# Optimization experiments

Measured on AMD Instinct MI355X. Metric: run time of the kernel, lower is better.

Reference implementation:

```python
import jax, jax.numpy as jnp
import numpy as np

H = 1024
NUM_HEADS = 16
HEAD_DIM = H // NUM_HEADS
EPS = 1e-6
GEN_E, GEN_IE = 8, 4096 // 8     # general experts, per-expert intermediate
MOD_E, MOD_IE = 4, 4096 // 4     # per-modality experts, per-expert intermediate


def layernorm(x, g, b):
    m = jnp.mean(x, axis=-1, keepdims=True)
    v = jnp.mean((x - m) ** 2, axis=-1, keepdims=True)
    return (x - m) * jax.lax.rsqrt(v + EPS) * g + b


def attention(x, qkv_w, qkv_b, proj_w, proj_b):
    B, N, _ = x.shape
    qkv = (x @ qkv_w + qkv_b).reshape(B, N, 3, NUM_HEADS, HEAD_DIM)
    qkv = jnp.transpose(qkv, (2, 0, 3, 1, 4))  # [3,B,h,N,d]
    q, k, v = qkv[0], qkv[1], qkv[2]
    scale = HEAD_DIM ** -0.5
    attn = jax.nn.softmax(jnp.einsum('bhnd,bhmd->bhnm', q, k) * scale, axis=-1)
    out = jnp.einsum('bhnm,bhmd->bhnd', attn, v)
    out = jnp.transpose(out, (0, 2, 1, 3)).reshape(B, N, H)
    return out @ proj_w + proj_b


def routed_mlp(x, position_ids, gate_up, down, ie):
    # expert_id = position % num_experts; compute all experts then select per token
    # (avoids materializing per-token [T,H,2I] gathered weights).
    E = gate_up.shape[0]
    eids = position_ids % E  # [B,N]
    gu = jnp.einsum('bnh,ehi->bnei', x, gate_up)              # [B,N,E,2*ie]
    gu = jnp.take_along_axis(gu, eids[..., None, None], axis=2)[:, :, 0]
    gate, up = gu[..., :ie], gu[..., ie:]
    inter = jax.nn.silu(gate) * up                             # [B,N,ie]
    dn = jnp.einsum('bni,eih->bneh', inter, down)              # [B,N,E,H]
    return jnp.take_along_axis(dn, eids[..., None, None], axis=2)[:, :, 0]


def setup_inputs() -> dict:
    key = jax.random.key(0)
    ks = jax.random.split(key, 16)
    B, N = 2, 2048
    inp = {
        'x': jax.random.normal(ks[0], (B, N, H), jnp.float32),
        'qkv_w': jax.random.normal(ks[1], (H, 3 * H), jnp.float32) * 0.02,
        'qkv_b': jnp.zeros((3 * H,), jnp.float32),
        'proj_w': jax.random.normal(ks[2], (H, H), jnp.float32) * 0.02,
        'proj_b': jnp.zeros((H,), jnp.float32),
        'ln1_g': jnp.ones((H,), jnp.float32), 'ln1_b': jnp.zeros((H,), jnp.float32),
        'ln2_g': jnp.ones((H,), jnp.float32), 'ln2_b': jnp.zeros((H,), jnp.float32),
        'ln3_g': jnp.ones((H,), jnp.float32), 'ln3_b': jnp.zeros((H,), jnp.float32),
        'gen_gu': jax.random.normal(ks[3], (GEN_E, H, 2 * GEN_IE), jnp.float32) * 0.02,
        'gen_dn': jax.random.normal(ks[4], (GEN_E, GEN_IE, H), jnp.float32) * 0.02,
        'text_gu': jax.random.normal(ks[5], (MOD_E, H, 2 * MOD_IE), jnp.float32) * 0.02,
        'text_dn': jax.random.normal(ks[6], (MOD_E, MOD_IE, H), jnp.float32) * 0.02,
        'img_gu': jax.random.normal(ks[7], (MOD_E, H, 2 * MOD_IE), jnp.float32) * 0.02,
        'img_dn': jax.random.normal(ks[8], (MOD_E, MOD_IE, H), jnp.float32) * 0.02,
        'aud_gu': jax.random.normal(ks[9], (MOD_E, H, 2 * MOD_IE), jnp.float32) * 0.02,
        'aud_dn': jax.random.normal(ks[10], (MOD_E, MOD_IE, H), jnp.float32) * 0.02,
        'vid_gu': jax.random.normal(ks[11], (MOD_E, H, 2 * MOD_IE), jnp.float32) * 0.02,
        'vid_dn': jax.random.normal(ks[12], (MOD_E, MOD_IE, H), jnp.float32) * 0.02,
        'modality_ids': jax.random.randint(ks[13], (B, N), 0, 4, jnp.int32),
        'position_ids': jnp.arange(B * N, dtype=jnp.int32).reshape(B, N),
    }
    return inp


def reference(x, qkv_w, qkv_b, proj_w, proj_b,
              ln1_g, ln1_b, ln2_g, ln2_b, ln3_g, ln3_b,
              gen_gu, gen_dn, text_gu, text_dn, img_gu, img_dn,
              aud_gu, aud_dn, vid_gu, vid_dn,
              modality_ids, position_ids):
    x = x + attention(layernorm(x, ln1_g, ln1_b), qkv_w, qkv_b, proj_w, proj_b)
    x = x + routed_mlp(layernorm(x, ln2_g, ln2_b), position_ids, gen_gu, gen_dn, GEN_IE)
    normed = layernorm(x, ln3_g, ln3_b)
    tm = (modality_ids == 0)[..., None].astype(x.dtype)
    im = (modality_ids == 1)[..., None].astype(x.dtype)
    am = (modality_ids == 2)[..., None].astype(x.dtype)
    vm = (modality_ids == 3)[..., None].astype(x.dtype)
    x = x + (routed_mlp(normed, position_ids, text_gu, text_dn, MOD_IE) * tm
             + routed_mlp(normed, position_ids, img_gu, img_dn, MOD_IE) * im
             + routed_mlp(normed, position_ids, aud_gu, aud_dn, MOD_IE) * am
             + routed_mlp(normed, position_ids, vid_gu, vid_dn, MOD_IE) * vm)
    return x
```

## Files before the change

### kernel.cpp

```cpp
#include <hip/hip_runtime.h>

#define T_TOKENS 4096
#define HDIM 1024

typedef __attribute__((ext_vector_type(8))) short bf16x8;
typedef __attribute__((ext_vector_type(4))) float f32x4;

#define EXP2F(x) __builtin_amdgcn_exp2f(x)

static __device__ inline unsigned short f2bf(float f) {
  unsigned u = __float_as_uint(f);
  unsigned r = (u + 0x7FFFu + ((u >> 16) & 1u)) >> 16;
  return (unsigned short)r;
}
static __device__ __forceinline__ unsigned cvtpk(float lo, float hi) {
  unsigned r;
  asm("v_cvt_pk_bf16_f32 %0, %1, %2" : "=v"(r) : "v"(lo), "v"(hi));
  return r;
}
static __device__ __forceinline__ void gl16(const void* g, void* l) {
  __builtin_amdgcn_global_load_lds((const __attribute__((address_space(1))) void*)g,
                                   (__attribute__((address_space(3))) void*)l, 16, 0, 0);
}

__launch_bounds__(256)
__global__ void ln_kernel(const float* __restrict__ in, const float* __restrict__ g,
                          const float* __restrict__ b, unsigned short* __restrict__ out) {
  const int row = blockIdx.x;
  const int tid = threadIdx.x;
  const long base = (long)row * HDIM;
  float4 v = *(const float4*)(in + base + tid * 4);
  __shared__ float red[256];
  red[tid] = v.x + v.y + v.z + v.w;
  __syncthreads();
  for (int st = 128; st > 0; st >>= 1) {
    if (tid < st) red[tid] += red[tid + st];
    __syncthreads();
  }
  const float mean = red[0] * (1.f / HDIM);
  __syncthreads();
  const float dx = v.x - mean, dy = v.y - mean, dz = v.z - mean, dw = v.w - mean;
  red[tid] = dx * dx + dy * dy + dz * dz + dw * dw;
  __syncthreads();
  for (int st = 128; st > 0; st >>= 1) {
    if (tid < st) red[tid] += red[tid + st];
    __syncthreads();
  }
  const float rstd = rsqrtf(red[0] * (1.f / HDIM) + 1e-6f);
  const int c = tid * 4;
  const float4 g4 = *(const float4*)(g + c);
  const float4 b4 = *(const float4*)(b + c);
  uint2 o;
  o.x = cvtpk(dx * rstd * g4.x + b4.x, dy * rstd * g4.y + b4.y);
  o.y = cvtpk(dz * rstd * g4.z + b4.z, dw * rstd * g4.w + b4.w);
  *(uint2*)(out + base + c) = o;
}

__launch_bounds__(256)
__global__ void build_groups(const int* __restrict__ pids, const int* __restrict__ mids,
                             int* __restrict__ gen_cnt, int* __restrict__ gen_list,
                             int* __restrict__ mod_cnt, int* __restrict__ mod_list) {
  const int t = blockIdx.x * 256 + threadIdx.x;
  if (t >= T_TOKENS) return;
  const int p = pids[t];
  const int ge = p & 7;
  int s = atomicAdd(&gen_cnt[ge], 1);
  if (s < 512) gen_list[ge * 512 + s] = t;
  const int g = mids[t] * 4 + (p & 3);
  s = atomicAdd(&mod_cnt[g], 1);
  if (s < 1024) mod_list[g * 1024 + s] = t;
}

__launch_bounds__(256)
__global__ void convert_w(const float* __restrict__ W, unsigned short* __restrict__ Wt,
                          int K, int N) {
  const long zo = (long)blockIdx.z * K * N;
  const float* Wp = W + zo;
  unsigned short* Wo = Wt + zo;
  const int n0 = blockIdx.x * 64, k0 = blockIdx.y * 64;
  __shared__ float T[64][65];
  const int tid = threadIdx.x;
#pragma unroll
  for (int i = 0; i < 4; ++i) {
    const int item = tid + i * 256;
    const int kk = item >> 4, c4 = (item & 15) * 4;
    const float4 v = *(const float4*)(Wp + (long)(k0 + kk) * N + n0 + c4);
    T[c4 + 0][kk] = v.x; T[c4 + 1][kk] = v.y; T[c4 + 2][kk] = v.z; T[c4 + 3][kk] = v.w;
  }
  __syncthreads();
#pragma unroll
  for (int i = 0; i < 4; ++i) {
    const int item = tid + i * 256;
    const int nn = item >> 4, k4 = (item & 15) * 4;
    uint2 p;
    p.x = cvtpk(T[nn][k4 + 0], T[nn][k4 + 1]);
    p.y = cvtpk(T[nn][k4 + 2], T[nn][k4 + 3]);
    *(uint2*)(Wo + (long)(n0 + nn) * K + k0 + k4) = p;
  }
}

enum { MODE_DENSE = 0, MODE_GEN = 1, MODE_MOD = 2 };
enum { OM_F32R = 0, OM_BF16 = 1, OM_QKV = 2 };

template <int MODE, int OMODE, bool WBF16, bool BIAS, int BM, int BN>
__launch_bounds__(256)
__global__ void mgemm(const unsigned short* __restrict__ A,
                      const void* __restrict__ w0, const float* __restrict__ w1,
                      const float* __restrict__ w2, const float* __restrict__ w3,
                      long wstep, const float* __restrict__ bias,
                      const float* __restrict__ resid, void* __restrict__ Cout,
                      unsigned short* __restrict__ qb, unsigned short* __restrict__ kb,
                      unsigned short* __restrict__ vtb,
                      int K, int N,
                      const int* __restrict__ cnts, const int* __restrict__ rowlist,
                      int cap) {
  const int z = blockIdx.z;
  const int n0 = blockIdx.x * BN;
  const int m0 = blockIdx.y * BM;

  int Meff = 1 << 30;
  const int* list = nullptr;
  if constexpr (MODE != MODE_DENSE) {
    Meff = cnts[z];
    if (m0 >= Meff) return;
    list = rowlist + z * cap;
  }

  constexpr int MR = BM / 32;
  constexpr int NR = BN / 32;
  constexpr int JB = BN / 32;
  constexpr int ABUF = BM * 128;
  constexpr int BBUF = BN * 128;
  __shared__ char As[2 * ABUF];
  __shared__ char Bs[2 * BBUF];

  const int tid = threadIdx.x;
  const int w = tid >> 6;
  const int lane = tid & 63;
  const int wm = w >> 1, wn = w & 1;
  const int srow = lane >> 3, sc = lane & 7;

  const unsigned short* asrc[MR];
#pragma unroll
  for (int i = 0; i < MR; ++i) {
    const int r = w * (BM / 4) + i * 8 + srow;
    long tok;
    if constexpr (MODE == MODE_DENSE) {
      tok = m0 + r;
    } else {
      int gm = m0 + r;
      if (gm >= Meff) gm = Meff - 1;
      tok = (long)list[gm];
    }
    asrc[i] = A + tok * (long)K + (sc ^ (r & 7)) * 8;
  }

  const unsigned short* bsrc[NR];
  const float* bptr[JB];
  int boff[JB];
  if constexpr (WBF16) {
    const unsigned short* W = (const unsigned short*)w0;
    if constexpr (MODE != MODE_DENSE) W += (long)z * wstep;
#pragma unroll
    for (int i = 0; i < NR; ++i) {
      const int r = w * (BN / 4) + i * 8 + srow;
      bsrc[i] = W + (long)(n0 + r) * K + (sc ^ (r & 7)) * 8;
    }
  } else {
    const float* W;
    if constexpr (MODE == MODE_MOD) {
      const int mm = z >> 2;
      const float* basep = (mm == 0) ? (const float*)w0 : (mm == 1) ? w1 : (mm == 2) ? w2 : w3;
      W = basep + (long)(z & 3) * wstep;
    } else {
      W = (const float*)w0 + (MODE != MODE_DENSE ? (long)z * wstep : 0);
    }
#pragma unroll
    for (int j = 0; j < JB; ++j) {
      const int item = tid + j * 256;
      const int kc = item / BN;
      const int nl = item % BN;
      bptr[j] = W + (long)(kc * 8) * N + n0 + nl;
      boff[j] = (nl * 128 + kc * 16) ^ ((nl & 7) << 4);
    }
  }

  f32x4 acc[MR][NR] = {};
  float kv[JB][8];

  auto stageA = [&](int s, int kt) {
#pragma unroll
    for (int i = 0; i < MR; ++i)
      gl16(asrc[i] + kt, As + s * ABUF + w * (BM * 32) + i * 1024);
  };
  auto stageB16 = [&](int s, int kt) {
#pragma unroll
    for (int i = 0; i < NR; ++i)
      gl16(bsrc[i] + kt, Bs + s * BBUF + w * (BN * 32) + i * 1024);
  };
  auto loadB = [&](int kt) {
#pragma unroll
    for (int j = 0; j < JB; ++j) {
      const float* bp = bptr[j] + (long)kt * N;
#pragma unroll
      for (int u = 0; u < 8; ++u) kv[j][u] = bp[(long)u * N];
    }
  };
  auto writeB = [&](int s) {
#pragma unroll
    for (int j = 0; j < JB; ++j) {
      uint4 p;
      p.x = cvtpk(kv[j][0], kv[j][1]);
      p.y = cvtpk(kv[j][2], kv[j][3]);
      p.z = cvtpk(kv[j][4], kv[j][5]);
      p.w = cvtpk(kv[j][6], kv[j][7]);
      *(uint4*)(Bs + s * BBUF + boff[j]) = p;
    }
  };
  auto compute = [&](int s) {
#pragma unroll
    for (int kk = 0; kk < 2; ++kk) {
      const int kb2 = kk * 64 + (lane >> 4) * 16;
      bf16x8 af[MR], bfr[NR];
#pragma unroll
      for (int f = 0; f < MR; ++f) {
        const int ar = wm * (BM / 2) + f * 16 + (lane & 15);
        af[f] = *(bf16x8*)(As + s * ABUF + ((ar * 128 + kb2) ^ ((ar & 7) << 4)));
      }
#pragma unroll
      for (int f = 0; f < NR; ++f) {
        const int br = wn * (BN / 2) + f * 16 + (lane & 15);
        bfr[f] = *(bf16x8*)(Bs + s * BBUF + ((br * 128 + kb2) ^ ((br & 7) << 4)));
      }
#pragma unroll
      for (int mf = 0; mf < MR; ++mf)
#pragma unroll
        for (int nf = 0; nf < NR; ++nf)
          acc[mf][nf] =
              __builtin_amdgcn_mfma_f32_16x16x32_bf16(af[mf], bfr[nf], acc[mf][nf], 0, 0, 0);
    }
  };

  const int nk = K >> 6;
  stageA(0, 0);
  if constexpr (WBF16) {
    stageB16(0, 0);
  } else {
    loadB(0);
    writeB(0);
  }
  __syncthreads();

  int sel = 0;
  for (int t = 0; t < nk; ++t) {
    const bool more = (t + 1) < nk;
    const int ktn = (t + 1) * 64;
    if (more) {
      stageA(sel ^ 1, ktn);
      if constexpr (WBF16) stageB16(sel ^ 1, ktn);
      else loadB(ktn);
    }
    compute(sel);
    if constexpr (!WBF16) {
      if (more) writeB(sel ^ 1);
    }
    __syncthreads();
    sel ^= 1;
  }

  const int lr4 = (lane >> 4) * 4;
  const int lc = lane & 15;
#pragma unroll
  for (int mf = 0; mf < MR; ++mf) {
#pragma unroll
    for (int r = 0; r < 4; ++r) {
      const int gm = m0 + wm * (BM / 2) + mf * 16 + lr4 + r;
      long orow;
      if constexpr (MODE == MODE_DENSE) {
        orow = gm;
      } else {
        if (gm >= Meff) continue;
        orow = (long)list[gm];
      }
#pragma unroll
      for (int nf = 0; nf < NR; ++nf) {
        const int gc = n0 + wn * (BN / 2) + nf * 16 + lc;
        float val = acc[mf][nf][r];
        if constexpr (BIAS) val += bias[gc];
        if constexpr (OMODE == OM_F32R) {
          val += resid[orow * (long)N + gc];
          ((float*)Cout)[orow * (long)N + gc] = val;
        } else if constexpr (OMODE == OM_BF16) {
          ((unsigned short*)Cout)[orow * (long)N + gc] = f2bf(val);
        } else {
          const int bb = (int)(orow >> 11), tl = (int)orow & 2047;
          const int seg = gc >> 10, hc = gc & 1023, h = hc >> 6, d = hc & 63;
          if (seg == 0)
            qb[(((long)(bb * 16 + h) * 2048) + tl) * 64 + d] = f2bf(val * 0.18033688011112042f);
          else if (seg == 1)
            kb[(((long)(bb * 16 + h) * 2048) + tl) * 64 + d] = f2bf(val);
          else
            vtb[((long)(bb * 16 + h) * 64 + d) * 2048 + tl] = f2bf(val);
        }
      }
    }
  }
}

__launch_bounds__(256)
__global__ void attn_kernel(const unsigned short* __restrict__ Qb,
                            const unsigned short* __restrict__ Kb,
                            const unsigned short* __restrict__ Vtb,
                            unsigned short* __restrict__ out) {
  const int lin = blockIdx.x + blockIdx.y * 16;
  const int xcd = lin & 7, rank = lin >> 3;
  const int bh = xcd * 4 + (rank >> 4);
  const int qt = rank & 15;
  const int b = bh >> 4, h = bh & 15;
  const int tid = threadIdx.x;
  const int w = tid >> 6;
  const int lane = tid & 63;
  const int g = lane >> 4;
  const int q = lane & 15;

  __shared__ char Ksb[128 * 128];
  __shared__ char Vsb[64 * 256];
  __shared__ char Psb[4 * 32 * 256];
  char* Pwb = Psb + w * 32 * 256;
  const int qx = q << 4;

  const unsigned short* Qh = Qb + ((long)(b * 16 + h) * 2048 + qt * 128) * 64;
  const unsigned short* Kh = Kb + (long)(b * 16 + h) * 2048 * 64;
  const unsigned short* Vh = Vtb + (long)(b * 16 + h) * 64 * 2048;

  bf16x8 qfA[2], qfB[2];
#pragma unroll
  for (int kst = 0; kst < 2; ++kst) {
    qfA[kst] = *(const bf16x8*)(Qh + (w * 32 + q) * 64 + kst * 32 + g * 8);
    qfB[kst] = *(const bf16x8*)(Qh + (w * 32 + 16 + q) * 64 + kst * 32 + g * 8);
  }

  const unsigned short* ksrc[4];
  const unsigned short* vsrc[4];
  char* kld = Ksb + w * 4096;
  char* vld = Vsb + w * 4096;
#pragma unroll
  for (int i = 0; i < 4; ++i) {
    const int r = w * 32 + i * 8 + (lane >> 3);
    ksrc[i] = Kh + (long)r * 64 + ((lane & 7) ^ (r & 7)) * 8;
    const int d = w * 16 + i * 4 + (lane >> 4);
    vsrc[i] = Vh + (long)d * 2048 + ((lane & 15) ^ (d & 7)) * 8;
  }

  float mA = -1e30f, lA = 0.f, mB = -1e30f, lB = 0.f;
  f32x4 accA[4] = {}, accB[4] = {};

  for (int kt = 0; kt < 16; ++kt) {
    __syncthreads();
#pragma unroll
    for (int i = 0; i < 4; ++i) gl16(ksrc[i] + (long)kt * 128 * 64, kld + i * 1024);
#pragma unroll
    for (int i = 0; i < 4; ++i) gl16(vsrc[i] + kt * 128, vld + i * 1024);
    __syncthreads();

    f32x4 sfA[8], sfB[8];
#pragma unroll
    for (int f = 0; f < 8; ++f) {
      const int krow = f * 16 + q;
      const int sw = (krow & 7) << 4;
      const bf16x8 k0 = *(bf16x8*)(Ksb + krow * 128 + ((g * 16) ^ sw));
      const bf16x8 k1 = *(bf16x8*)(Ksb + krow * 128 + ((64 + g * 16) ^ sw));
      f32x4 tA = {};
      tA = __builtin_amdgcn_mfma_f32_16x16x32_bf16(k0, qfA[0], tA, 0, 0, 0);
      sfA[f] = __builtin_amdgcn_mfma_f32_16x16x32_bf16(k1, qfA[1], tA, 0, 0, 0);
      f32x4 tB = {};
      tB = __builtin_amdgcn_mfma_f32_16x16x32_bf16(k0, qfB[0], tB, 0, 0, 0);
      sfB[f] = __builtin_amdgcn_mfma_f32_16x16x32_bf16(k1, qfB[1], tB, 0, 0, 0);
    }

    {
      float pm = fmaxf(fmaxf(sfA[0][0], sfA[0][1]), fmaxf(sfA[0][2], sfA[0][3]));
#pragma unroll
      for (int f = 1; f < 8; ++f)
        pm = fmaxf(pm, fmaxf(fmaxf(sfA[f][0], sfA[f][1]), fmaxf(sfA[f][2], sfA[f][3])));
      pm = fmaxf(pm, __shfl_xor(pm, 16));
      pm = fmaxf(pm, __shfl_xor(pm, 32));
      float al = 1.f;
      if (!__all(pm - mA <= 8.f)) {
        const float mn = fmaxf(mA, pm);
        al = EXP2F(mA - mn);
        mA = mn;
#pragma unroll
        for (int r = 0; r < 4; ++r) {
          const float aO = __shfl(al, g * 4 + r, 64);
          accA[0][r] *= aO; accA[1][r] *= aO; accA[2][r] *= aO; accA[3][r] *= aO;
        }
      }
      float ls = 0.f;
#pragma unroll
      for (int f = 0; f < 8; ++f) {
#pragma unroll
        for (int r = 0; r < 4; ++r) sfA[f][r] = EXP2F(sfA[f][r] - mA);
        ls += (sfA[f][0] + sfA[f][1]) + (sfA[f][2] + sfA[f][3]);
      }
      ls += __shfl_xor(ls, 16);
      ls += __shfl_xor(ls, 32);
      lA = lA * al + ls;
    }
    {
      float pm = fmaxf(fmaxf(sfB[0][0], sfB[0][1]), fmaxf(sfB[0][2], sfB[0][3]));
#pragma unroll
      for (int f = 1; f < 8; ++f)
        pm = fmaxf(pm, fmaxf(fmaxf(sfB[f][0], sfB[f][1]), fmaxf(sfB[f][2], sfB[f][3])));
      pm = fmaxf(pm, __shfl_xor(pm, 16));
      pm = fmaxf(pm, __shfl_xor(pm, 32));
      float al = 1.f;
      if (!__all(pm - mB <= 8.f)) {
        const float mn = fmaxf(mB, pm);
        al = EXP2F(mB - mn);
        mB = mn;
#pragma unroll
        for (int r = 0; r < 4; ++r) {
          const float aO = __shfl(al, g * 4 + r, 64);
          accB[0][r] *= aO; accB[1][r] *= aO; accB[2][r] *= aO; accB[3][r] *= aO;
        }
      }
      float ls = 0.f;
#pragma unroll
      for (int f = 0; f < 8; ++f) {
#pragma unroll
        for (int r = 0; r < 4; ++r) sfB[f][r] = EXP2F(sfB[f][r] - mB);
        ls += (sfB[f][0] + sfB[f][1]) + (sfB[f][2] + sfB[f][3]);
      }
      ls += __shfl_xor(ls, 16);
      ls += __shfl_xor(ls, 32);
      lB = lB * al + ls;
    }

#pragma unroll
    for (int f = 0; f < 8; ++f) {
      const int col = (f * 32 + g * 8) ^ qx;
      uint2 pA; pA.x = cvtpk(sfA[f][0], sfA[f][1]); pA.y = cvtpk(sfA[f][2], sfA[f][3]);
      *(uint2*)(Pwb + q * 256 + col) = pA;
      uint2 pB; pB.x = cvtpk(sfB[f][0], sfB[f][1]); pB.y = cvtpk(sfB[f][2], sfB[f][3]);
      *(uint2*)(Pwb + (q + 16) * 256 + col) = pB;
    }

#pragma unroll
    for (int kst = 0; kst < 4; ++kst) {
      const int pcol = (kst * 64 + g * 16) ^ qx;
      const bf16x8 paA = *(bf16x8*)(Pwb + q * 256 + pcol);
      const bf16x8 paB = *(bf16x8*)(Pwb + (q + 16) * 256 + pcol);
#pragma unroll
      for (int df = 0; df < 4; ++df) {
        const int vrow = df * 16 + q;
        const int vsw = (vrow & 7) << 4;
        const bf16x8 vf = *(bf16x8*)(Vsb + vrow * 256 + ((kst * 64 + g * 16) ^ vsw));
        accA[df] = __builtin_amdgcn_mfma_f32_16x16x32_bf16(paA, vf, accA[df], 0, 0, 0);
        accB[df] = __builtin_amdgcn_mfma_f32_16x16x32_bf16(paB, vf, accB[df], 0, 0, 0);
      }
    }
  }

  float liA[4], liB[4];
#pragma unroll
  for (int r = 0; r < 4; ++r) {
    liA[r] = 1.f / __shfl(lA, g * 4 + r, 64);
    liB[r] = 1.f / __shfl(lB, g * 4 + r, 64);
  }
  unsigned short* opA = out + (long)(b * 2048 + qt * 128 + w * 32) * 1024 + h * 64;
  unsigned short* opB = opA + 16 * 1024;
#pragma unroll
  for (int df = 0; df < 4; ++df)
#pragma unroll
    for (int r = 0; r < 4; ++r) {
      const int row = g * 4 + r;
      opA[(long)row * 1024 + df * 16 + q] = f2bf(accA[df][r] * liA[r]);
      opB[(long)row * 1024 + df * 16 + q] = f2bf(accB[df][r] * liB[r]);
    }
}

__launch_bounds__(256)
__global__ void silu_bf(const unsigned short* __restrict__ gu, unsigned short* __restrict__ inter,
                        int IE2, int IE, int shift) {
  const int total = T_TOKENS << shift;
  for (int idx = blockIdx.x * 256 + threadIdx.x; idx < total; idx += gridDim.x * 256) {
    const int t = idx >> shift;
    const int r8 = (idx & ((1 << shift) - 1)) * 8;
    const unsigned short* gp = gu + (long)t * IE2 + r8;
    const uint4 gg = *(const uint4*)gp;
    const uint4 uu = *(const uint4*)(gp + IE);
    const unsigned gw[4] = {gg.x, gg.y, gg.z, gg.w};
    const unsigned uw[4] = {uu.x, uu.y, uu.z, uu.w};
    uint4 o;
    unsigned ow[4];
#pragma unroll
    for (int qq = 0; qq < 4; ++qq) {
      const float g0 = __uint_as_float(gw[qq] << 16);
      const float g1 = __uint_as_float(gw[qq] & 0xffff0000u);
      const float u0 = __uint_as_float(uw[qq] << 16);
      const float u1 = __uint_as_float(uw[qq] & 0xffff0000u);
      const float r0 = g0 / (1.f + __expf(-g0)) * u0;
      const float r1 = g1 / (1.f + __expf(-g1)) * u1;
      ow[qq] = cvtpk(r0, r1);
    }
    o.x = ow[0]; o.y = ow[1]; o.z = ow[2]; o.w = ow[3];
    *(uint4*)(inter + (long)t * IE + r8) = o;
  }
}

extern "C" void kernel_launch(void* const* d_in, const int* in_sizes, int n_in,
                              void* d_out, int out_size, void* d_ws, size_t ws_size,
                              hipStream_t stream) {
  const float* x       = (const float*)d_in[0];
  const float* qkv_w   = (const float*)d_in[1];
  const float* qkv_b   = (const float*)d_in[2];
  const float* proj_w  = (const float*)d_in[3];
  const float* proj_b  = (const float*)d_in[4];
  const float* ln1_g   = (const float*)d_in[5];
  const float* ln1_b   = (const float*)d_in[6];
  const float* ln2_g   = (const float*)d_in[7];
  const float* ln2_b   = (const float*)d_in[8];
  const float* ln3_g   = (const float*)d_in[9];
  const float* ln3_b   = (const float*)d_in[10];
  const float* gen_gu  = (const float*)d_in[11];
  const float* gen_dn  = (const float*)d_in[12];
  const float* text_gu = (const float*)d_in[13];
  const float* text_dn = (const float*)d_in[14];
  const float* img_gu  = (const float*)d_in[15];
  const float* img_dn  = (const float*)d_in[16];
  const float* aud_gu  = (const float*)d_in[17];
  const float* aud_dn  = (const float*)d_in[18];
  const float* vid_gu  = (const float*)d_in[19];
  const float* vid_dn  = (const float*)d_in[20];
  const int* mids      = (const int*)d_in[21];
  const int* pids      = (const int*)d_in[22];
  float* out = (float*)d_out;
  char* ws = (char*)d_ws;

  const unsigned long MB = 1ul << 20;
  unsigned short* lnb   = (unsigned short*)(ws);
  unsigned short* Qb    = (unsigned short*)(ws + 8 * MB);
  unsigned short* Kb    = (unsigned short*)(ws + 16 * MB);
  unsigned short* Vtb   = (unsigned short*)(ws + 24 * MB);
  unsigned short* attno = (unsigned short*)(ws + 32 * MB);
  unsigned short* wqkv  = (unsigned short*)(ws + 40 * MB);
  unsigned short* wproj = (unsigned short*)(ws + 46 * MB);
  unsigned short* wggu  = (unsigned short*)(ws + 48 * MB);
  unsigned short* wgdn  = (unsigned short*)(ws + 64 * MB);
  int* gen_cnt  = (int*)(ws + 72 * MB);
  int* mod_cnt  = gen_cnt + 8;
  int* gen_list = gen_cnt + 32;
  int* mod_list = gen_list + 8 * 512;
  unsigned short* guo    = Qb;
  unsigned short* intero = Vtb;

  (void)hipMemsetAsync(gen_cnt, 0, (8 + 16) * sizeof(int), stream);
  build_groups<<<16, 256, 0, stream>>>(pids, mids, gen_cnt, gen_list, mod_cnt, mod_list);

  convert_w<<<dim3(48, 16, 1), 256, 0, stream>>>(qkv_w, wqkv, 1024, 3072);
  convert_w<<<dim3(16, 16, 1), 256, 0, stream>>>(proj_w, wproj, 1024, 1024);
  convert_w<<<dim3(16, 16, 8), 256, 0, stream>>>(gen_gu, wggu, 1024, 1024);
  convert_w<<<dim3(16, 8, 8), 256, 0, stream>>>(gen_dn, wgdn, 512, 1024);

  ln_kernel<<<4096, 256, 0, stream>>>(x, ln1_g, ln1_b, lnb);
  mgemm<MODE_DENSE, OM_QKV, true, true, 128, 128><<<dim3(24, 32, 1), 256, 0, stream>>>(
      lnb, wqkv, nullptr, nullptr, nullptr, 0L, qkv_b, nullptr, nullptr,
      Qb, Kb, Vtb, 1024, 3072, nullptr, nullptr, 0);
  attn_kernel<<<dim3(16, 32, 1), 256, 0, stream>>>(Qb, Kb, Vtb, attno);
  mgemm<MODE_DENSE, OM_F32R, true, true, 128, 128><<<dim3(8, 32, 1), 256, 0, stream>>>(
      attno, wproj, nullptr, nullptr, nullptr, 0L, proj_b, x, out,
      nullptr, nullptr, nullptr, 1024, 1024, nullptr, nullptr, 0);

  ln_kernel<<<4096, 256, 0, stream>>>(out, ln2_g, ln2_b, lnb);
  mgemm<MODE_GEN, OM_BF16, true, false, 128, 128><<<dim3(8, 4, 8), 256, 0, stream>>>(
      lnb, wggu, nullptr, nullptr, nullptr, (long)1024 * 1024, nullptr, nullptr, guo,
      nullptr, nullptr, nullptr, 1024, 1024, gen_cnt, gen_list, 512);
  silu_bf<<<1024, 256, 0, stream>>>(guo, intero, 1024, 512, 6);
  mgemm<MODE_GEN, OM_F32R, true, false, 128, 128><<<dim3(8, 4, 8), 256, 0, stream>>>(
      intero, wgdn, nullptr, nullptr, nullptr, (long)1024 * 512, nullptr, out, out,
      nullptr, nullptr, nullptr, 512, 1024, gen_cnt, gen_list, 512);

  ln_kernel<<<4096, 256, 0, stream>>>(out, ln3_g, ln3_b, lnb);
  mgemm<MODE_MOD, OM_BF16, false, false, 128, 128><<<dim3(16, 8, 16), 256, 0, stream>>>(
      lnb, text_gu, img_gu, aud_gu, vid_gu, (long)1024 * 2048, nullptr, nullptr, guo,
      nullptr, nullptr, nullptr, 1024, 2048, mod_cnt, mod_list, 1024);
  silu_bf<<<2048, 256, 0, stream>>>(guo, intero, 2048, 1024, 7);
  mgemm<MODE_MOD, OM_F32R, false, false, 128, 128><<<dim3(8, 8, 16), 256, 0, stream>>>(
      intero, text_dn, img_dn, aud_dn, vid_dn, (long)1024 * 1024, nullptr, out, out,
      nullptr, nullptr, nullptr, 1024, 1024, mod_cnt, mod_list, 1024);
}
```

Baseline: 388.2 us.

## Stage fp32 weights via coalesced float4 loads and LDS transpose, narrow modality GEMM tiles

For the fp32-weight GEMM path, each thread now loads contiguous float4 rows of the weight tile into a raw LDS buffer, then transposes and converts to bf16 from LDS. This replaces the earlier strided per-element global loads, which were poorly coalesced. The modality-expert GEMMs also switch to BN=64 tiles with twice as many blocks. The cost is an extra LDS round trip, an additional __syncthreads per k-step, and about 17KB more shared memory.

```diff
diff --git a/kernel.cpp b/kernel.cpp
--- a/kernel.cpp
+++ b/kernel.cpp
@@ -129,10 +129,12 @@
   constexpr int MR = BM / 32;
   constexpr int NR = BN / 32;
   constexpr int JB = BN / 32;
+  constexpr int RAWP = (BN * 64) / 1024;
   constexpr int ABUF = BM * 128;
   constexpr int BBUF = BN * 128;
   __shared__ char As[2 * ABUF];
   __shared__ char Bs[2 * BBUF];
+  __shared__ char Braw[WBF16 ? 16 : 64 * 272];
 
   const int tid = threadIdx.x;
   const int w = tid >> 6;
@@ -156,8 +158,8 @@
   }
 
   const unsigned short* bsrc[NR];
-  const float* bptr[JB];
-  int boff[JB];
+  const float* wcol = nullptr;
+  int rk[4], rn[4];
   if constexpr (WBF16) {
     const unsigned short* W = (const unsigned short*)w0;
     if constexpr (MODE != MODE_DENSE) W += (long)z * wstep;
@@ -175,46 +177,54 @@
     } else {
       W = (const float*)w0 + (MODE != MODE_DENSE ? (long)z * wstep : 0);
     }
+    wcol = W + n0;
+#pragma unroll
+    for (int p = 0; p < RAWP; ++p) {
+      const int item = tid + p * 256;
+      rk[p] = item >> (BN == 64 ? 4 : 5);
+      rn[p] = (item & (BN / 4 - 1)) * 4;
+    }
+  }
+
+  f32x4 acc[MR][NR] = {};
+  float4 braw[RAWP];
+
+  auto stageA = [&](int s, int kt) {
+#pragma unroll
+    for (int i = 0; i < MR; ++i)
+      gl16(asrc[i] + kt, As + s * ABUF + w * (BM * 32) + i * 1024);
+  };
+  auto stageB16 = [&](int s, int kt) {
+#pragma unroll
+    for (int i = 0; i < NR; ++i)
+      gl16(bsrc[i] + kt, Bs + s * BBUF + w * (BN * 32) + i * 1024);
+  };
+  auto loadRaw = [&](int kt) {
+#pragma unroll
+    for (int p = 0; p < RAWP; ++p)
+      braw[p] = *(const float4*)(wcol + (long)(kt + rk[p]) * N + rn[p]);
+  };
+  auto writeRaw = [&]() {
+#pragma unroll
+    for (int p = 0; p < RAWP; ++p)
+      *(float4*)(Braw + rk[p] * 272 + rn[p] * 4) = braw[p];
+  };
+  auto transposeB = [&](int s) {
 #pragma unroll
     for (int j = 0; j < JB; ++j) {
       const int item = tid + j * 256;
       const int kc = item / BN;
       const int nl = item % BN;
-      bptr[j] = W + (long)(kc * 8) * N + n0 + nl;
-      boff[j] = (nl * 128 + kc * 16) ^ ((nl & 7) << 4);
-    }
-  }
-
-  f32x4 acc[MR][NR] = {};
-  float kv[JB][8];
-
-  auto stageA = [&](int s, int kt) {
-#pragma unroll
-    for (int i = 0; i < MR; ++i)
-      gl16(asrc[i] + kt, As + s * ABUF + w * (BM * 32) + i * 1024);
-  };
-  auto stageB16 = [&](int s, int kt) {
-#pragma unroll
-    for (int i = 0; i < NR; ++i)
-      gl16(bsrc[i] + kt, Bs + s * BBUF + w * (BN * 32) + i * 1024);
-  };
-  auto loadB = [&](int kt) {
-#pragma unroll
-    for (int j = 0; j < JB; ++j) {
-      const float* bp = bptr[j] + (long)kt * N;
-#pragma unroll
-      for (int u = 0; u < 8; ++u) kv[j][u] = bp[(long)u * N];
-    }
-  };
-  auto writeB = [&](int s) {
-#pragma unroll
-    for (int j = 0; j < JB; ++j) {
+      float v[8];
+#pragma unroll
+      for (int u = 0; u < 8; ++u)
+        v[u] = *(const float*)(Braw + (kc * 8 + u) * 272 + nl * 4);
       uint4 p;
-      p.x = cvtpk(kv[j][0], kv[j][1]);
-      p.y = cvtpk(kv[j][2], kv[j][3]);
-      p.z = cvtpk(kv[j][4], kv[j][5]);
-      p.w = cvtpk(kv[j][6], kv[j][7]);
-      *(uint4*)(Bs + s * BBUF + boff[j]) = p;
+      p.x = cvtpk(v[0], v[1]);
+      p.y = cvtpk(v[2], v[3]);
+      p.z = cvtpk(v[4], v[5]);
+      p.w = cvtpk(v[6], v[7]);
+      *(uint4*)(Bs + s * BBUF + ((nl * 128 + kc * 16) ^ ((nl & 7) << 4))) = p;
     }
   };
   auto compute = [&](int s) {
@@ -242,30 +252,43 @@
   };
 
   const int nk = K >> 6;
-  stageA(0, 0);
+  int sel = 0;
   if constexpr (WBF16) {
+    stageA(0, 0);
     stageB16(0, 0);
+    __syncthreads();
+    for (int t = 0; t < nk; ++t) {
+      const bool more = (t + 1) < nk;
+      const int ktn = (t + 1) * 64;
+      if (more) {
+        stageA(sel ^ 1, ktn);
+        stageB16(sel ^ 1, ktn);
+      }
+      compute(sel);
+      __syncthreads();
+      sel ^= 1;
+    }
   } else {
-    loadB(0);
-    writeB(0);
-  }
-  __syncthreads();
-
-  int sel = 0;
-  for (int t = 0; t < nk; ++t) {
-    const bool more = (t + 1) < nk;
-    const int ktn = (t + 1) * 64;
-    if (more) {
-      stageA(sel ^ 1, ktn);
-      if constexpr (WBF16) stageB16(sel ^ 1, ktn);
-      else loadB(ktn);
-    }
-    compute(sel);
-    if constexpr (!WBF16) {
-      if (more) writeB(sel ^ 1);
-    }
+    stageA(0, 0);
+    loadRaw(0);
+    writeRaw();
     __syncthreads();
-    sel ^= 1;
+    transposeB(0);
+    __syncthreads();
+    for (int t = 0; t < nk; ++t) {
+      const bool more = (t + 1) < nk;
+      const int ktn = (t + 1) * 64;
+      if (more) {
+        stageA(sel ^ 1, ktn);
+        loadRaw(ktn);
+      }
+      compute(sel);
+      if (more) writeRaw();
+      __syncthreads();
+      if (more) transposeB(sel ^ 1);
+      __syncthreads();
+      sel ^= 1;
+    }
   }
 
   const int lr4 = (lane >> 4) * 4;
@@ -582,11 +605,11 @@
       nullptr, nullptr, nullptr, 512, 1024, gen_cnt, gen_list, 512);
 
   ln_kernel<<<4096, 256, 0, stream>>>(out, ln3_g, ln3_b, lnb);
-  mgemm<MODE_MOD, OM_BF16, false, false, 128, 128><<<dim3(16, 8, 16), 256, 0, stream>>>(
+  mgemm<MODE_MOD, OM_BF16, false, false, 128, 64><<<dim3(32, 8, 16), 256, 0, stream>>>(
       lnb, text_gu, img_gu, aud_gu, vid_gu, (long)1024 * 2048, nullptr, nullptr, guo,
       nullptr, nullptr, nullptr, 1024, 2048, mod_cnt, mod_list, 1024);
   silu_bf<<<2048, 256, 0, stream>>>(guo, intero, 2048, 1024, 7);
-  mgemm<MODE_MOD, OM_F32R, false, false, 128, 128><<<dim3(8, 8, 16), 256, 0, stream>>>(
+  mgemm<MODE_MOD, OM_F32R, false, false, 128, 64><<<dim3(16, 8, 16), 256, 0, stream>>>(
       intero, text_dn, img_dn, aud_dn, vid_dn, (long)1024 * 1024, nullptr, out, out,
       nullptr, nullptr, nullptr, 1024, 1024, mod_cnt, mod_list, 1024);
 }
```

Measured after the change: 510.8 us. 31.6% more time.
